# Kernel optimization log

Measured on AMD Instinct MI355X. Metric: run time of the kernel, lower is better.

The kernel has to match this reference:

```python
import jax, jax.numpy as jnp
import numpy as np

B, N, C, DK, TOPK = 4, 4096, 256, 64, 8


def setup_inputs() -> dict:
    key = jax.random.key(0)
    k1, k2, k3 = jax.random.split(key, 3)
    x = jax.random.normal(k1, (B, N, C), dtype=jnp.float32)
    # nn.Linear(channels, d_k, bias=False) weights, stored as [C, DK] for x @ W
    W_q = jax.random.normal(k2, (C, DK), dtype=jnp.float32) * (C ** -0.5)
    W_k = jax.random.normal(k3, (C, DK), dtype=jnp.float32) * (C ** -0.5)
    return {"x": x, "W_q": W_q, "W_k": W_k, "top_k": TOPK}


def reference(x, W_q, W_k, top_k):
    d_k = W_q.shape[-1]
    scale = d_k ** -0.5
    Q = x @ W_q                                   # [B, N, DK]
    K = x @ W_k                                   # [B, N, DK]
    S = jnp.einsum('bnd,bmd->bnm', Q, K) * scale  # [B, N, N]
    _, topk_idx = jax.lax.top_k(S, top_k)         # [B, N, top_k]
    n = S.shape[-1]
    # scatter True at top-k column indices per row (mirrors torch scatter_)
    row_mask = lambda idx: jnp.zeros((n,), dtype=bool).at[idx].set(True)
    mask = jax.vmap(jax.vmap(row_mask))(topk_idx)  # [B, N, N] bool
    S_masked = jnp.where(mask, S, -jnp.inf)
    A = jax.nn.softmax(S_masked, axis=-1)
    return A
```

## Files before the change

### kernel.cpp

```cpp
#include <hip/hip_runtime.h>
#include <math.h>

#define NROW 16384
#define NCOL 4096
#define CDIM 256
#define DKDIM 64
#define SCALE 0.125f

typedef float v4f __attribute__((ext_vector_type(4)));
typedef __attribute__((ext_vector_type(8))) short short8v;
typedef __attribute__((ext_vector_type(4))) float f32x4;

__device__ __forceinline__ unsigned mono(float v) {
  unsigned u = __float_as_uint(v);
  unsigned s = (unsigned)(((int)u) >> 31);
  return u ^ (s | 0x80000000u);
}
__device__ __forceinline__ float unmono(unsigned k) {
  unsigned u = (k & 0x80000000u) ? (k ^ 0x80000000u) : ~k;
  return __uint_as_float(u);
}
__device__ __forceinline__ unsigned short f2bf(float f) {
  unsigned u = __float_as_uint(f);
  u += 0x7FFFu + ((u >> 16) & 1u);
  return (unsigned short)(u >> 16);
}
__device__ __forceinline__ unsigned umaxu(unsigned a, unsigned b) { return a > b ? a : b; }

__device__ __forceinline__ void ins8(unsigned tk[8], unsigned& tmin, int& tmpos, unsigned v) {
  #pragma unroll
  for (int j = 0; j < 8; ++j) if (j == tmpos) tk[j] = v;
  tmin = tk[0]; tmpos = 0;
  #pragma unroll
  for (int j = 1; j < 8; ++j) if (tk[j] < tmin) { tmin = tk[j]; tmpos = j; }
}
__device__ __forceinline__ unsigned umax8(const unsigned kv[8]) {
  unsigned a = umaxu(umaxu(kv[0], kv[1]), umaxu(kv[2], kv[3]));
  unsigned b = umaxu(umaxu(kv[4], kv[5]), umaxu(kv[6], kv[7]));
  return umaxu(a, b);
}
__device__ __forceinline__ void seed8r(const unsigned kv[8],
                                       unsigned tk[8], unsigned& tmin, int& tmpos) {
  #pragma unroll
  for (int j = 0; j < 8; ++j) tk[j] = kv[j];
  tmin = tk[0]; tmpos = 0;
  #pragma unroll
  for (int j = 1; j < 8; ++j) if (tk[j] < tmin) { tmin = tk[j]; tmpos = j; }
}
__device__ __forceinline__ void scan8r(const unsigned kvin[8],
                                       unsigned tk[8], unsigned& tmin, int& tmpos) {
  unsigned kv[8];
  #pragma unroll
  for (int j = 0; j < 8; ++j) kv[j] = kvin[j];
  unsigned gm = umax8(kv);
  #pragma unroll
  for (int pass = 0; pass < 2; ++pass) {
    if (__any(gm > tmin)) {
      if (gm > tmin) {
        ins8(tk, tmin, tmpos, gm);
        #pragma unroll
        for (int j = 0; j < 8; ++j) if (kv[j] == gm) kv[j] = 0u;
      }
      gm = umax8(kv);
    }
  }
  if (__any(gm > tmin)) {
    #pragma unroll
    for (int j = 0; j < 8; ++j) if (kv[j] > tmin) ins8(tk, tmin, tmpos, kv[j]);
  }
}
__device__ __forceinline__ void seed8(const unsigned* __restrict__ sp,
                                      unsigned tk[8], unsigned& tmin, int& tmpos) {
  uint4 ka = *(const uint4*)(sp);
  uint4 kb = *(const uint4*)(sp + 4);
  unsigned kv[8] = {ka.x, ka.y, ka.z, ka.w, kb.x, kb.y, kb.z, kb.w};
  seed8r(kv, tk, tmin, tmpos);
}
__device__ __forceinline__ void scan8(const unsigned* __restrict__ sp,
                                      unsigned tk[8], unsigned& tmin, int& tmpos) {
  uint4 ka = *(const uint4*)(sp);
  uint4 kb = *(const uint4*)(sp + 4);
  unsigned kv[8] = {ka.x, ka.y, ka.z, ka.w, kb.x, kb.y, kb.z, kb.w};
  scan8r(kv, tk, tmin, tmpos);
}

__global__ __launch_bounds__(512, 2) void qk_proj(
    const float* __restrict__ x, const float* __restrict__ Wq,
    const float* __restrict__ Wk, float* __restrict__ Qt,
    float* __restrict__ Kt, unsigned short* __restrict__ Qh,
    unsigned short* __restrict__ Kh) {
  __shared__ float4 xs4[64][65];
  const int t = threadIdx.x;
  const int rb = blockIdx.x;
  {
    const float4* xg = (const float4*)(x + (size_t)rb * 64 * CDIM);
    #pragma unroll
    for (int i = 0; i < 8; ++i) {
      int idx = i * 512 + t;
      xs4[idx >> 6][idx & 63] = xg[idx];
    }
  }
  __syncthreads();

  const int lane = t & 63;
  const int wu = __builtin_amdgcn_readfirstlane(t >> 6);
  const int proj = wu >> 2;
  const int chunk = wu & 3;
  const float* __restrict__ Wp = proj ? Wk : Wq;

  float acc[16];
  #pragma unroll
  for (int j = 0; j < 16; ++j) acc[j] = 0.f;

  #pragma unroll 4
  for (int cs = 0; cs < 64; ++cs) {
    float4 xv = xs4[lane][cs];
    const float xc[4] = {xv.x, xv.y, xv.z, xv.w};
    #pragma unroll
    for (int i = 0; i < 4; ++i) {
      const float4* __restrict__ w4 =
          (const float4*)(Wp + (size_t)(cs * 4 + i) * DKDIM + chunk * 16);
      float4 wa = w4[0], wb = w4[1], wc = w4[2], wd = w4[3];
      float xi = xc[i];
      acc[0]  = fmaf(xi, wa.x, acc[0]);  acc[1]  = fmaf(xi, wa.y, acc[1]);
      acc[2]  = fmaf(xi, wa.z, acc[2]);  acc[3]  = fmaf(xi, wa.w, acc[3]);
      acc[4]  = fmaf(xi, wb.x, acc[4]);  acc[5]  = fmaf(xi, wb.y, acc[5]);
      acc[6]  = fmaf(xi, wb.z, acc[6]);  acc[7]  = fmaf(xi, wb.w, acc[7]);
      acc[8]  = fmaf(xi, wc.x, acc[8]);  acc[9]  = fmaf(xi, wc.y, acc[9]);
      acc[10] = fmaf(xi, wc.z, acc[10]); acc[11] = fmaf(xi, wc.w, acc[11]);
      acc[12] = fmaf(xi, wd.x, acc[12]); acc[13] = fmaf(xi, wd.y, acc[13]);
      acc[14] = fmaf(xi, wd.z, acc[14]); acc[15] = fmaf(xi, wd.w, acc[15]);
    }
  }

  const int gr = rb * 64 + lane;
  float* Of = (proj ? Kt : Qt) + (size_t)gr * 64 + chunk * 16;
  #pragma unroll
  for (int i = 0; i < 4; ++i) {
    float4 o = {acc[4 * i], acc[4 * i + 1], acc[4 * i + 2], acc[4 * i + 3]};
    ((float4*)Of)[i] = o;
  }
  unsigned short* Oh = (proj ? Kh : Qh) + (size_t)gr * 64 + chunk * 16;
  unsigned hp[8];
  #pragma unroll
  for (int i = 0; i < 8; ++i)
    hp[i] = (unsigned)f2bf(acc[2 * i]) | ((unsigned)f2bf(acc[2 * i + 1]) << 16);
  uint4 h0 = {hp[0], hp[1], hp[2], hp[3]};
  uint4 h1 = {hp[4], hp[5], hp[6], hp[7]};
  ((uint4*)Oh)[0] = h0;
  ((uint4*)Oh)[1] = h1;
}

__global__ __launch_bounds__(256, 4) void s_cand(
    const unsigned short* __restrict__ Qh, const unsigned short* __restrict__ Kh,
    unsigned* __restrict__ wsk) {
  __shared__ unsigned keys[4][16 * 132];
  const int t = threadIdx.x;
  const int lane = t & 63;
  const int w = __builtin_amdgcn_readfirstlane(t >> 6);
  const int f = blockIdx.x;
  const int xs = f & 7;
  const int i5 = f >> 3;
  const int combo = xs * 4 + (i5 >> 6);
  const int rbL = i5 & 63;
  const int b = combo >> 3;
  const int chunk = combo & 7;

  const int l15 = lane & 15, lk = lane >> 4;
  const int rowg = (b << 12) + rbL * 64 + w * 16 + l15;
  const short8v a0 = *(const short8v*)(Qh + (size_t)rowg * 64 + lk * 8);
  const short8v a1 = *(const short8v*)(Qh + (size_t)rowg * 64 + lk * 8 + 32);

  const unsigned short* Kb = Kh + ((size_t)(b << 12)) * 64;

  unsigned tk[4][8]; unsigned tmin[4]; int tmpos[4];

  #pragma unroll 1
  for (int g = 0; g < 4; ++g) {
    unsigned kv[4][8];
    #pragma unroll
    for (int t8 = 0; t8 < 8; ++t8) {
      const int ct = g * 8 + t8;
      const int col = chunk * 512 + ct * 16 + l15;
      const unsigned short* kp = Kb + (size_t)col * 64 + lk * 8;
      const short8v b0 = *(const short8v*)(kp);
      const short8v b1 = *(const short8v*)(kp + 32);
      f32x4 acc = {0.f, 0.f, 0.f, 0.f};
      acc = __builtin_amdgcn_mfma_f32_16x16x32_bf16(a0, b0, acc, 0, 0, 0);
      acc = __builtin_amdgcn_mfma_f32_16x16x32_bf16(a1, b1, acc, 0, 0, 0);
      #pragma unroll
      for (int i = 0; i < 4; ++i)
        kv[i][t8] = (mono(acc[i]) & 0xFFFFF000u) | (unsigned)col;
    }
    if (g == 0) {
      #pragma unroll
      for (int i = 0; i < 4; ++i) seed8r(kv[i], tk[i], tmin[i], tmpos[i]);
    } else {
      #pragma unroll
      for (int i = 0; i < 4; ++i) scan8r(kv[i], tk[i], tmin[i], tmpos[i]);
    }
  }

  unsigned* krow = keys[w];
  #pragma unroll
  for (int i = 0; i < 4; ++i) {
    uint4 s0 = {tk[i][0], tk[i][1], tk[i][2], tk[i][3]};
    uint4 s1 = {tk[i][4], tk[i][5], tk[i][6], tk[i][7]};
    uint4* mp4 = (uint4*)(krow + (lk * 4 + i) * 132 + l15 * 8);
    mp4[0] = s0; mp4[1] = s1;
  }
  const int myrow = lane >> 2, q = lane & 3;
  unsigned mt[8]; unsigned mmin; int mmpos;
  {
    const unsigned* sp = krow + myrow * 132 + q * 32;
    seed8(sp, mt, mmin, mmpos);
    scan8(sp + 8, mt, mmin, mmpos);
    scan8(sp + 16, mt, mmin, mmpos);
    scan8(sp + 24, mt, mmin, mmpos);
  }
  {
    uint4 s0 = {mt[0], mt[1], mt[2], mt[3]};
    uint4 s1 = {mt[4], mt[5], mt[6], mt[7]};
    uint4* mp4 = (uint4*)(krow + myrow * 36 + q * 8);
    mp4[0] = s0; mp4[1] = s1;
  }
  if (lane < 16) {
    const unsigned* mp = krow + lane * 36;
    unsigned ft[8]; unsigned fmin; int fmpos;
    seed8(mp, ft, fmin, fmpos);
    scan8(mp + 8, ft, fmin, fmpos);
    scan8(mp + 16, ft, fmin, fmpos);
    scan8(mp + 24, ft, fmin, fmpos);
    const int grow = (b << 12) + rbL * 64 + w * 16 + lane;
    uint4 o0 = {ft[0], ft[1], ft[2], ft[3]};
    uint4 o1 = {ft[4], ft[5], ft[6], ft[7]};
    uint4* wp = (uint4*)(wsk + (size_t)grow * 64 + chunk * 8);
    wp[0] = o0; wp[1] = o1;
  }
}

__global__ __launch_bounds__(256) void finalize(
    const float* __restrict__ Qt, const float* __restrict__ Kt,
    const unsigned* __restrict__ wsk, float* __restrict__ out) {
  const int t = threadIdx.x;
  const int lane = t & 63;
  const int w = t >> 6;
  const int row = blockIdx.x * 4 + w;
  const int b = row >> 12;
  const unsigned key = wsk[(size_t)row * 64 + lane];
  const int col = (int)(key & 0xFFFu);
  const float4* Kp = (const float4*)(Kt + ((size_t)((b << 12) + col)) * 64);
  const float4* Qp = (const float4*)(Qt + (size_t)row * 64);
  float s = 0.f;
  #pragma unroll
  for (int g = 0; g < 16; ++g) {
    float4 qf = Qp[g];
    float4 kf = Kp[g];
    s = fmaf(qf.x, kf.x, s);
    s = fmaf(qf.y, kf.y, s);
    s = fmaf(qf.z, kf.z, s);
    s = fmaf(qf.w, kf.w, s);
  }
  unsigned kx = mono(s);
  float vals[8]; int cols[8];
  #pragma unroll
  for (int it = 0; it < 8; ++it) {
    unsigned m = kx;
    #pragma unroll
    for (int d = 1; d < 64; d <<= 1) m = umaxu(m, (unsigned)__shfl_xor((int)m, d, 64));
    unsigned long long win = __ballot(kx == m);
    int wl = (int)__ffsll(win) - 1;
    cols[it] = __shfl(col, wl, 64);
    vals[it] = unmono(m);
    if (lane == wl) kx = 0u;
  }
  float vq[8]; float sum = 0.f;
  #pragma unroll
  for (int it = 0; it < 8; ++it) { vq[it] = __expf((vals[it] - vals[0]) * SCALE); sum += vq[it]; }
  float inv = 1.f / sum;
  #pragma unroll
  for (int it = 0; it < 8; ++it) vq[it] *= inv;

  v4f* orow4 = (v4f*)(out + ((size_t)row << 12));
  #pragma unroll
  for (int i = 0; i < 16; ++i) {
    const int base = i * 256 + lane * 4;
    v4f z = {0.f, 0.f, 0.f, 0.f};
    #pragma unroll
    for (int q = 0; q < 8; ++q) {
      z.x = (cols[q] == base)     ? vq[q] : z.x;
      z.y = (cols[q] == base + 1) ? vq[q] : z.y;
      z.z = (cols[q] == base + 2) ? vq[q] : z.z;
      z.w = (cols[q] == base + 3) ? vq[q] : z.w;
    }
    __builtin_nontemporal_store(z, &orow4[(size_t)i * 64 + lane]);
  }
}

extern "C" void kernel_launch(void* const* d_in, const int* in_sizes, int n_in,
                              void* d_out, int out_size, void* d_ws, size_t ws_size,
                              hipStream_t stream) {
  const float* x  = (const float*)d_in[0];
  const float* Wq = (const float*)d_in[1];
  const float* Wk = (const float*)d_in[2];
  float* out = (float*)d_out;

  char* ws = (char*)d_ws;
  float* Qt = (float*)ws;
  float* Kt = (float*)(ws + ((size_t)4 << 20));
  unsigned short* Qh = (unsigned short*)(ws + ((size_t)8 << 20));
  unsigned short* Kh = (unsigned short*)(ws + ((size_t)10 << 20));
  unsigned* wsk = (unsigned*)(ws + ((size_t)12 << 20));

  qk_proj<<<dim3(NROW / 64), 512, 0, stream>>>(x, Wq, Wk, Qt, Kt, Qh, Kh);
  s_cand<<<2048, 256, 0, stream>>>(Qh, Kh, wsk);
  finalize<<<NROW / 4, 256, 0, stream>>>(Qt, Kt, wsk, out);
}
```

Measured before the change: 469.2 us.

## Fuse candidate top-k scan and finalize softmax/scatter into one kernel

Merges the bf16 MFMA candidate-selection kernel and the fp32 rescoring/softmax/output kernel into a single kernel. Each 256-thread block now handles 32 rows, with two waves per 16-row group splitting the columns in halves. Candidates are merged in shared memory instead of going through a global workspace. This removes a launch and the global candidate round-trip, but leaves only 512 blocks, each doing a longer serial column loop, which may reduce parallelism and latency hiding.

```diff
diff --git a/kernel.cpp b/kernel.cpp
--- a/kernel.cpp
+++ b/kernel.cpp
@@ -151,37 +151,39 @@
   ((uint4*)Oh)[1] = h1;
 }
 
-__global__ __launch_bounds__(256, 4) void s_cand(
+__global__ __launch_bounds__(256, 2) void s_fused(
     const unsigned short* __restrict__ Qh, const unsigned short* __restrict__ Kh,
-    unsigned* __restrict__ wsk) {
-  __shared__ unsigned keys[4][16 * 132];
+    const float* __restrict__ Qt, const float* __restrict__ Kt,
+    float* __restrict__ out) {
+  __shared__ unsigned keys[32 * 260];
+  __shared__ unsigned cand[32][64];
+  __shared__ float    pval[32][8];
+  __shared__ int      pcol[32][8];
+
   const int t = threadIdx.x;
   const int lane = t & 63;
-  const int w = __builtin_amdgcn_readfirstlane(t >> 6);
-  const int f = blockIdx.x;
-  const int xs = f & 7;
-  const int i5 = f >> 3;
-  const int combo = xs * 4 + (i5 >> 6);
-  const int rbL = i5 & 63;
-  const int b = combo >> 3;
-  const int chunk = combo & 7;
+  const int wu = __builtin_amdgcn_readfirstlane(t >> 6);
+  const int rg = wu >> 1;
+  const int h = wu & 1;
+  const int bid = blockIdx.x;
+  const int orig = (bid & 7) * 64 + (bid >> 3);
+  const int blockrow = orig * 32;
+  const int b = blockrow >> 12;
 
   const int l15 = lane & 15, lk = lane >> 4;
-  const int rowg = (b << 12) + rbL * 64 + w * 16 + l15;
+  const int rowg = blockrow + rg * 16 + l15;
   const short8v a0 = *(const short8v*)(Qh + (size_t)rowg * 64 + lk * 8);
   const short8v a1 = *(const short8v*)(Qh + (size_t)rowg * 64 + lk * 8 + 32);
 
   const unsigned short* Kb = Kh + ((size_t)(b << 12)) * 64;
 
   unsigned tk[4][8]; unsigned tmin[4]; int tmpos[4];
-
   #pragma unroll 1
-  for (int g = 0; g < 4; ++g) {
+  for (int g = 0; g < 16; ++g) {
     unsigned kv[4][8];
     #pragma unroll
     for (int t8 = 0; t8 < 8; ++t8) {
-      const int ct = g * 8 + t8;
-      const int col = chunk * 512 + ct * 16 + l15;
+      const int col = h * 2048 + (g * 8 + t8) * 16 + l15;
       const unsigned short* kp = Kb + (size_t)col * 64 + lk * 8;
       const short8v b0 = *(const short8v*)(kp);
       const short8v b1 = *(const short8v*)(kp + 32);
@@ -200,100 +202,91 @@
       for (int i = 0; i < 4; ++i) scan8r(kv[i], tk[i], tmin[i], tmpos[i]);
     }
   }
-
-  unsigned* krow = keys[w];
   #pragma unroll
   for (int i = 0; i < 4; ++i) {
+    unsigned* kr = keys + (rg * 16 + lk * 4 + i) * 260 + h * 128 + l15 * 8;
     uint4 s0 = {tk[i][0], tk[i][1], tk[i][2], tk[i][3]};
     uint4 s1 = {tk[i][4], tk[i][5], tk[i][6], tk[i][7]};
-    uint4* mp4 = (uint4*)(krow + (lk * 4 + i) * 132 + l15 * 8);
-    mp4[0] = s0; mp4[1] = s1;
-  }
-  const int myrow = lane >> 2, q = lane & 3;
-  unsigned mt[8]; unsigned mmin; int mmpos;
+    ((uint4*)kr)[0] = s0; ((uint4*)kr)[1] = s1;
+  }
+  __syncthreads();
+
   {
-    const unsigned* sp = krow + myrow * 132 + q * 32;
+    const int row = t >> 3, q = t & 7;
+    const unsigned* sp = keys + row * 260 + q * 32;
+    unsigned mt[8]; unsigned mmin; int mmpos;
     seed8(sp, mt, mmin, mmpos);
     scan8(sp + 8, mt, mmin, mmpos);
     scan8(sp + 16, mt, mmin, mmpos);
     scan8(sp + 24, mt, mmin, mmpos);
-  }
-  {
-    uint4 s0 = {mt[0], mt[1], mt[2], mt[3]};
-    uint4 s1 = {mt[4], mt[5], mt[6], mt[7]};
-    uint4* mp4 = (uint4*)(krow + myrow * 36 + q * 8);
-    mp4[0] = s0; mp4[1] = s1;
-  }
-  if (lane < 16) {
-    const unsigned* mp = krow + lane * 36;
-    unsigned ft[8]; unsigned fmin; int fmpos;
-    seed8(mp, ft, fmin, fmpos);
-    scan8(mp + 8, ft, fmin, fmpos);
-    scan8(mp + 16, ft, fmin, fmpos);
-    scan8(mp + 24, ft, fmin, fmpos);
-    const int grow = (b << 12) + rbL * 64 + w * 16 + lane;
-    uint4 o0 = {ft[0], ft[1], ft[2], ft[3]};
-    uint4 o1 = {ft[4], ft[5], ft[6], ft[7]};
-    uint4* wp = (uint4*)(wsk + (size_t)grow * 64 + chunk * 8);
-    wp[0] = o0; wp[1] = o1;
-  }
-}
-
-__global__ __launch_bounds__(256) void finalize(
-    const float* __restrict__ Qt, const float* __restrict__ Kt,
-    const unsigned* __restrict__ wsk, float* __restrict__ out) {
-  const int t = threadIdx.x;
-  const int lane = t & 63;
-  const int w = t >> 6;
-  const int row = blockIdx.x * 4 + w;
-  const int b = row >> 12;
-  const unsigned key = wsk[(size_t)row * 64 + lane];
-  const int col = (int)(key & 0xFFFu);
-  const float4* Kp = (const float4*)(Kt + ((size_t)((b << 12) + col)) * 64);
-  const float4* Qp = (const float4*)(Qt + (size_t)row * 64);
-  float s = 0.f;
-  #pragma unroll
-  for (int g = 0; g < 16; ++g) {
-    float4 qf = Qp[g];
-    float4 kf = Kp[g];
-    s = fmaf(qf.x, kf.x, s);
-    s = fmaf(qf.y, kf.y, s);
-    s = fmaf(qf.z, kf.z, s);
-    s = fmaf(qf.w, kf.w, s);
-  }
-  unsigned kx = mono(s);
-  float vals[8]; int cols[8];
-  #pragma unroll
-  for (int it = 0; it < 8; ++it) {
-    unsigned m = kx;
-    #pragma unroll
-    for (int d = 1; d < 64; d <<= 1) m = umaxu(m, (unsigned)__shfl_xor((int)m, d, 64));
-    unsigned long long win = __ballot(kx == m);
-    int wl = (int)__ffsll(win) - 1;
-    cols[it] = __shfl(col, wl, 64);
-    vals[it] = unmono(m);
-    if (lane == wl) kx = 0u;
-  }
-  float vq[8]; float sum = 0.f;
-  #pragma unroll
-  for (int it = 0; it < 8; ++it) { vq[it] = __expf((vals[it] - vals[0]) * SCALE); sum += vq[it]; }
-  float inv = 1.f / sum;
-  #pragma unroll
-  for (int it = 0; it < 8; ++it) vq[it] *= inv;
-
-  v4f* orow4 = (v4f*)(out + ((size_t)row << 12));
-  #pragma unroll
-  for (int i = 0; i < 16; ++i) {
-    const int base = i * 256 + lane * 4;
-    v4f z = {0.f, 0.f, 0.f, 0.f};
-    #pragma unroll
-    for (int q = 0; q < 8; ++q) {
-      z.x = (cols[q] == base)     ? vq[q] : z.x;
-      z.y = (cols[q] == base + 1) ? vq[q] : z.y;
-      z.z = (cols[q] == base + 2) ? vq[q] : z.z;
-      z.w = (cols[q] == base + 3) ? vq[q] : z.w;
-    }
-    __builtin_nontemporal_store(z, &orow4[(size_t)i * 64 + lane]);
+    uint4 o0 = {mt[0], mt[1], mt[2], mt[3]};
+    uint4 o1 = {mt[4], mt[5], mt[6], mt[7]};
+    uint4* cp = (uint4*)(&cand[row][q * 8]);
+    cp[0] = o0; cp[1] = o1;
+  }
+  __syncthreads();
+
+  #pragma unroll 1
+  for (int p = 0; p < 8; ++p) {
+    const int rr = p * 4 + wu;
+    const unsigned key = cand[rr][lane];
+    const int col = (int)(key & 0xFFFu);
+    const float4* Kp = (const float4*)(Kt + ((size_t)((b << 12) + col)) * 64);
+    const float4* Qp = (const float4*)(Qt + (size_t)(blockrow + rr) * 64);
+    float s = 0.f;
+    #pragma unroll
+    for (int g2 = 0; g2 < 16; ++g2) {
+      float4 qf = Qp[g2];
+      float4 kf = Kp[g2];
+      s = fmaf(qf.x, kf.x, s);
+      s = fmaf(qf.y, kf.y, s);
+      s = fmaf(qf.z, kf.z, s);
+      s = fmaf(qf.w, kf.w, s);
+    }
+    unsigned kx = mono(s);
+    float vals[8]; int cols[8];
+    #pragma unroll
+    for (int it = 0; it < 8; ++it) {
+      unsigned m = kx;
+      #pragma unroll
+      for (int d = 1; d < 64; d <<= 1) m = umaxu(m, (unsigned)__shfl_xor((int)m, d, 64));
+      unsigned long long win = __ballot(kx == m);
+      int wl = (int)__ffsll(win) - 1;
+      cols[it] = __shfl(col, wl, 64);
+      vals[it] = unmono(m);
+      if (lane == wl) kx = 0u;
+    }
+    float vq[8]; float sum = 0.f;
+    #pragma unroll
+    for (int it = 0; it < 8; ++it) { vq[it] = __expf((vals[it] - vals[0]) * SCALE); sum += vq[it]; }
+    float inv = 1.f / sum;
+    if (lane < 8) {
+      pval[rr][lane] = vq[lane] * inv;
+      pcol[rr][lane] = cols[lane];
+    }
+  }
+  __syncthreads();
+
+  #pragma unroll 1
+  for (int j = 0; j < 8; ++j) {
+    const int sr = wu * 8 + j;
+    float vq[8]; int cols[8];
+    #pragma unroll
+    for (int q2 = 0; q2 < 8; ++q2) { vq[q2] = pval[sr][q2]; cols[q2] = pcol[sr][q2]; }
+    v4f* orow4 = (v4f*)(out + ((size_t)(blockrow + sr) << 12));
+    #pragma unroll
+    for (int i = 0; i < 16; ++i) {
+      const int base = i * 256 + lane * 4;
+      v4f z = {0.f, 0.f, 0.f, 0.f};
+      #pragma unroll
+      for (int q2 = 0; q2 < 8; ++q2) {
+        z.x = (cols[q2] == base)     ? vq[q2] : z.x;
+        z.y = (cols[q2] == base + 1) ? vq[q2] : z.y;
+        z.z = (cols[q2] == base + 2) ? vq[q2] : z.z;
+        z.w = (cols[q2] == base + 3) ? vq[q2] : z.w;
+      }
+      __builtin_nontemporal_store(z, &orow4[(size_t)i * 64 + lane]);
+    }
   }
 }
 
@@ -310,9 +303,7 @@
   float* Kt = (float*)(ws + ((size_t)4 << 20));
   unsigned short* Qh = (unsigned short*)(ws + ((size_t)8 << 20));
   unsigned short* Kh = (unsigned short*)(ws + ((size_t)10 << 20));
-  unsigned* wsk = (unsigned*)(ws + ((size_t)12 << 20));
 
   qk_proj<<<dim3(NROW / 64), 512, 0, stream>>>(x, Wq, Wk, Qt, Kt, Qh, Kh);
-  s_cand<<<2048, 256, 0, stream>>>(Qh, Kh, wsk);
-  finalize<<<NROW / 4, 256, 0, stream>>>(Qt, Kt, wsk, out);
-}
+  s_fused<<<512, 256, 0, stream>>>(Qh, Kh, Qt, Kt, out);
+}
```

Measured after the change: 448.6 us, median of 2. -4.4%, faster.
